# Optimization experiments

Measured on AMD Instinct MI355X. Metric: run time of the kernel, lower is better.

## Reference

```python
import jax, jax.numpy as jnp
import numpy as np

DIM = 1024
NUM_HEADS = 16
NUM_KV_HEADS = 4
HEAD_DIM = DIM // NUM_HEADS  # 64
QK_GAIN = 1.5
ROPE_BASE = 10000.0


def _rms_norm(x, eps):
    # F.rms_norm with no weight: x / sqrt(mean(x^2) + eps)
    ms = jnp.mean(jnp.square(x), axis=-1, keepdims=True)
    return x * jax.lax.rsqrt(ms + eps)


def _rope_tables(seqlen, dim, dtype):
    inv_freq = 1.0 / (ROPE_BASE ** (jnp.arange(0, dim, 2, dtype=jnp.float32) / dim))
    freqs = jnp.outer(jnp.arange(seqlen, dtype=jnp.float32), inv_freq)  # [N, D/2]
    emb = jnp.concatenate([freqs, freqs], axis=-1)  # [N, D]
    return jnp.cos(emb).astype(dtype), jnp.sin(emb).astype(dtype)


def _apply_rope(x, cos, sin):
    # x: [B, N, H, D]; cos/sin: [N, D] broadcast over batch and heads
    half = x.shape[-1] // 2
    rot = jnp.concatenate([-x[..., half:], x[..., :half]], axis=-1)
    return x * cos[None, :, None, :] + rot * sin[None, :, None, :]


def setup_inputs() -> dict:
    key = jax.random.key(0)
    ks = jax.random.split(key, 5)
    B, N, C = 4, 2048, DIM
    s = 0.02
    return {
        "x": jax.random.normal(ks[0], (B, N, C), dtype=jnp.float32),
        "wq": jax.random.normal(ks[1], (C, C), dtype=jnp.float32) * s,
        "wk": jax.random.normal(ks[2], (C, NUM_KV_HEADS * HEAD_DIM), dtype=jnp.float32) * s,
        "wv": jax.random.normal(ks[3], (C, NUM_KV_HEADS * HEAD_DIM), dtype=jnp.float32) * s,
        "wo": jax.random.normal(ks[4], (C, C), dtype=jnp.float32) * s,
    }


def reference(x, wq, wk, wv, wo) -> jnp.ndarray:
    B, N, C = x.shape
    H, Hkv, D = NUM_HEADS, NUM_KV_HEADS, HEAD_DIM
    eps = jnp.finfo(x.dtype).eps

    q = (x @ wq).reshape(B, N, H, D)
    k = (x @ wk).reshape(B, N, Hkv, D)
    v = (x @ wv).reshape(B, N, Hkv, D)

    q = _rms_norm(q, eps)
    k = _rms_norm(k, eps)

    cos, sin = _rope_tables(N, D, q.dtype)
    q = _apply_rope(q, cos, sin) * QK_GAIN
    k = _apply_rope(k, cos, sin)

    # GQA head expansion (repeat_interleave along head dim)
    g = H // Hkv
    k = jnp.repeat(k, g, axis=2)  # [B, N, H, D]
    v = jnp.repeat(v, g, axis=2)

    # causal SDPA, scale = 1/sqrt(D)
    scores = jnp.einsum("bqhd,bkhd->bhqk", q, k) / jnp.sqrt(jnp.asarray(D, q.dtype))
    causal = jnp.tril(jnp.ones((N, N), dtype=bool))
    scores = jnp.where(causal[None, None], scores, jnp.finfo(scores.dtype).min)
    probs = jax.nn.softmax(scores, axis=-1)
    y = jnp.einsum("bhqk,bkhd->bqhd", probs, v).reshape(B, N, C)
    return y @ wo
```

## Files before the change

### kernel.cpp

```cpp
#include <hip/hip_runtime.h>

typedef __bf16 bf16;
typedef __bf16 bf16x8 __attribute__((ext_vector_type(8)));
typedef __bf16 bf16x4 __attribute__((ext_vector_type(4)));
typedef float f32x4 __attribute__((ext_vector_type(4)));

#define B_ 4
#define N_ 2048
#define C_ 1024
#define H_ 16
#define HKV_ 4
#define D_ 64

#define QSCALE 0.2705053201666806f
#define NEGINF (-1.0e30f)

__global__ __launch_bounds__(256) void prep_qkv(const float* __restrict__ wq,
                                                const float* __restrict__ wk,
                                                const float* __restrict__ wv,
                                                bf16* __restrict__ wT) {
  __shared__ __align__(16) bf16 lds[64 * 72];
  int bx = blockIdx.x;
  const float* w;
  int ncols, tk, tn, nbase;
  if (bx < 256) {
    w = wq; ncols = 1024; tk = bx >> 4; tn = bx & 15; nbase = 0;
  } else if (bx < 320) {
    int t = bx - 256;
    w = wk; ncols = 256; tk = t >> 2; tn = t & 3; nbase = 1024;
  } else {
    int t = bx - 320;
    w = wv; ncols = 256; tk = t >> 2; tn = t & 3; nbase = 1280;
  }
  int tid = threadIdx.x;
#pragma unroll
  for (int i = 0; i < 4; ++i) {
    int c = tid + i * 256;
    int kr = c >> 4, n4 = (c & 15) * 4;
    f32x4 v = *(const f32x4*)(w + (size_t)(tk * 64 + kr) * ncols + tn * 64 + n4);
    bf16x4 b;
#pragma unroll
    for (int j = 0; j < 4; ++j) b[j] = (bf16)v[j];
    *(bf16x4*)(lds + kr * 72 + n4) = b;
  }
  __syncthreads();
#pragma unroll
  for (int i = 0; i < 2; ++i) {
    int c = tid + i * 256;
    int n = c >> 3, koff = (c & 7) * 8;
    bf16x8 tv;
#pragma unroll
    for (int j = 0; j < 8; ++j) tv[j] = lds[(koff + j) * 72 + n];
    *(bf16x8*)(wT + (size_t)(nbase + tn * 64 + n) * 1024 + tk * 64 + koff) = tv;
  }
}

__global__ __launch_bounds__(256) void prep_wo(const float* __restrict__ w,
                                               bf16* __restrict__ wT) {
  __shared__ __align__(16) bf16 lds[64 * 72];
  int tk = blockIdx.x >> 4, tn = blockIdx.x & 15;
  int tid = threadIdx.x;
#pragma unroll
  for (int i = 0; i < 4; ++i) {
    int c = tid + i * 256;
    int kr = c >> 4, n4 = (c & 15) * 4;
    f32x4 v = *(const f32x4*)(w + (size_t)(tk * 64 + kr) * 1024 + tn * 64 + n4);
    bf16x4 b;
#pragma unroll
    for (int j = 0; j < 4; ++j) b[j] = (bf16)v[j];
    *(bf16x4*)(lds + kr * 72 + n4) = b;
  }
  __syncthreads();
#pragma unroll
  for (int i = 0; i < 2; ++i) {
    int c = tid + i * 256;
    int n = c >> 3, koff = (c & 7) * 8;
    bf16x8 tv;
#pragma unroll
    for (int j = 0; j < 8; ++j) tv[j] = lds[(koff + j) * 72 + n];
    *(bf16x8*)(wT + (size_t)(tn * 64 + n) * 1024 + tk * 64 + koff) = tv;
  }
}

__global__ __launch_bounds__(256) void gemm_qkv(const float* __restrict__ x,
                                                const bf16* __restrict__ wT,
                                                bf16* __restrict__ qb,
                                                bf16* __restrict__ kvb) {
  __shared__ __align__(16) bf16 As[128 * 72];
  __shared__ __align__(16) bf16 Bs[128 * 72];
  int by = blockIdx.y;
  int n0 = by * 128;
  bf16* Out;
  int ostride, ocol0;
  if (by < 8) {
    Out = qb; ostride = 1024; ocol0 = by * 128;
  } else if (by < 10) {
    Out = kvb; ostride = 512; ocol0 = (by - 8) * 128;
  } else {
    Out = kvb; ostride = 512; ocol0 = 256 + (by - 10) * 128;
  }
  int m0 = blockIdx.x * 128;
  int tid = threadIdx.x;
  int wave = tid >> 6, lane = tid & 63;
  int quad = lane >> 4, lr = lane & 15;
  int wr = (wave >> 1) * 64, wc = (wave & 1) * 64;
  int arow = tid >> 4, aoff = (tid & 15) * 4;
  int brow = tid >> 3, boff = (tid & 7) * 8;

  f32x4 acc[4][4];
  const f32x4 z = {0.f, 0.f, 0.f, 0.f};
#pragma unroll
  for (int i = 0; i < 4; ++i)
#pragma unroll
    for (int j = 0; j < 4; ++j) acc[i][j] = z;

  f32x4 sa[8];
  bf16x8 sb[4];
#pragma unroll
  for (int i = 0; i < 8; ++i)
    sa[i] = *(const f32x4*)(x + (size_t)(m0 + arow + i * 16) * 1024 + aoff);
#pragma unroll
  for (int i = 0; i < 4; ++i)
    sb[i] = *(const bf16x8*)(wT + (size_t)(n0 + brow + i * 32) * 1024 + boff);
#pragma unroll
  for (int i = 0; i < 8; ++i) {
    bf16x4 a16;
#pragma unroll
    for (int j = 0; j < 4; ++j) a16[j] = (bf16)sa[i][j];
    *(bf16x4*)(As + (arow + i * 16) * 72 + aoff) = a16;
  }
#pragma unroll
  for (int i = 0; i < 4; ++i) *(bf16x8*)(Bs + (brow + i * 32) * 72 + boff) = sb[i];
  asm volatile("s_waitcnt lgkmcnt(0)" ::: "memory");
  __builtin_amdgcn_s_barrier();
  __builtin_amdgcn_sched_barrier(0);

  for (int k0 = 0; k0 < 1024; k0 += 64) {
    bool pf = (k0 + 64 < 1024);
    if (pf) {
#pragma unroll
      for (int i = 0; i < 8; ++i)
        sa[i] = *(const f32x4*)(x + (size_t)(m0 + arow + i * 16) * 1024 + k0 + 64 + aoff);
#pragma unroll
      for (int i = 0; i < 4; ++i)
        sb[i] = *(const bf16x8*)(wT + (size_t)(n0 + brow + i * 32) * 1024 + k0 + 64 + boff);
    }
#pragma unroll
    for (int kx = 0; kx < 2; ++kx) {
      bf16x8 af[4], bfr[4];
#pragma unroll
      for (int t = 0; t < 4; ++t) {
        af[t] = *(const bf16x8*)(As + (wr + t * 16 + lr) * 72 + kx * 32 + quad * 8);
        bfr[t] = *(const bf16x8*)(Bs + (wc + t * 16 + lr) * 72 + kx * 32 + quad * 8);
      }
      __builtin_amdgcn_s_setprio(1);
#pragma unroll
      for (int rt = 0; rt < 4; ++rt)
#pragma unroll
        for (int ct = 0; ct < 4; ++ct)
          acc[rt][ct] = __builtin_amdgcn_mfma_f32_16x16x32_bf16(af[rt], bfr[ct],
                                                                acc[rt][ct], 0, 0, 0);
      __builtin_amdgcn_s_setprio(0);
    }
    __builtin_amdgcn_s_barrier();
    __builtin_amdgcn_sched_barrier(0);
    if (pf) {
#pragma unroll
      for (int i = 0; i < 8; ++i) {
        bf16x4 a16;
#pragma unroll
        for (int j = 0; j < 4; ++j) a16[j] = (bf16)sa[i][j];
        *(bf16x4*)(As + (arow + i * 16) * 72 + aoff) = a16;
      }
#pragma unroll
      for (int i = 0; i < 4; ++i) *(bf16x8*)(Bs + (brow + i * 32) * 72 + boff) = sb[i];
      asm volatile("s_waitcnt lgkmcnt(0)" ::: "memory");
    }
    __builtin_amdgcn_s_barrier();
    __builtin_amdgcn_sched_barrier(0);
  }
#pragma unroll
  for (int rt = 0; rt < 4; ++rt)
#pragma unroll
    for (int ct = 0; ct < 4; ++ct)
#pragma unroll
      for (int r = 0; r < 4; ++r) {
        int row = m0 + wr + rt * 16 + quad * 4 + r;
        int col = ocol0 + wc + ct * 16 + lr;
        Out[(size_t)row * ostride + col] = (bf16)acc[rt][ct][r];
      }
}

__global__ __launch_bounds__(256) void gemm_out(const bf16* __restrict__ A,
                                                const bf16* __restrict__ Bt,
                                                float* __restrict__ C) {
  __shared__ __align__(16) bf16 As[128 * 72];
  __shared__ __align__(16) bf16 Bs[128 * 72];
  int m0 = blockIdx.x * 128, n0 = blockIdx.y * 128;
  int tid = threadIdx.x;
  int wave = tid >> 6, lane = tid & 63;
  int quad = lane >> 4, lr = lane & 15;
  int wr = (wave >> 1) * 64, wc = (wave & 1) * 64;
  int brow = tid >> 3, boff = (tid & 7) * 8;

  f32x4 acc[4][4];
  const f32x4 z = {0.f, 0.f, 0.f, 0.f};
#pragma unroll
  for (int i = 0; i < 4; ++i)
#pragma unroll
    for (int j = 0; j < 4; ++j) acc[i][j] = z;

  bf16x8 sa[4], sb[4];
#pragma unroll
  for (int i = 0; i < 4; ++i) {
    sa[i] = *(const bf16x8*)(A + (size_t)(m0 + brow + i * 32) * 1024 + boff);
    sb[i] = *(const bf16x8*)(Bt + (size_t)(n0 + brow + i * 32) * 1024 + boff);
  }
#pragma unroll
  for (int i = 0; i < 4; ++i) {
    *(bf16x8*)(As + (brow + i * 32) * 72 + boff) = sa[i];
    *(bf16x8*)(Bs + (brow + i * 32) * 72 + boff) = sb[i];
  }
  asm volatile("s_waitcnt lgkmcnt(0)" ::: "memory");
  __builtin_amdgcn_s_barrier();
  __builtin_amdgcn_sched_barrier(0);

  for (int k0 = 0; k0 < 1024; k0 += 64) {
    bool pf = (k0 + 64 < 1024);
    if (pf) {
#pragma unroll
      for (int i = 0; i < 4; ++i) {
        sa[i] = *(const bf16x8*)(A + (size_t)(m0 + brow + i * 32) * 1024 + k0 + 64 + boff);
        sb[i] = *(const bf16x8*)(Bt + (size_t)(n0 + brow + i * 32) * 1024 + k0 + 64 + boff);
      }
    }
#pragma unroll
    for (int kx = 0; kx < 2; ++kx) {
      bf16x8 af[4], bfr[4];
#pragma unroll
      for (int t = 0; t < 4; ++t) {
        af[t] = *(const bf16x8*)(As + (wr + t * 16 + lr) * 72 + kx * 32 + quad * 8);
        bfr[t] = *(const bf16x8*)(Bs + (wc + t * 16 + lr) * 72 + kx * 32 + quad * 8);
      }
      __builtin_amdgcn_s_setprio(1);
#pragma unroll
      for (int rt = 0; rt < 4; ++rt)
#pragma unroll
        for (int ct = 0; ct < 4; ++ct)
          acc[rt][ct] = __builtin_amdgcn_mfma_f32_16x16x32_bf16(af[rt], bfr[ct],
                                                                acc[rt][ct], 0, 0, 0);
      __builtin_amdgcn_s_setprio(0);
    }
    __builtin_amdgcn_s_barrier();
    __builtin_amdgcn_sched_barrier(0);
    if (pf) {
#pragma unroll
      for (int i = 0; i < 4; ++i) {
        *(bf16x8*)(As + (brow + i * 32) * 72 + boff) = sa[i];
        *(bf16x8*)(Bs + (brow + i * 32) * 72 + boff) = sb[i];
      }
      asm volatile("s_waitcnt lgkmcnt(0)" ::: "memory");
    }
    __builtin_amdgcn_s_barrier();
    __builtin_amdgcn_sched_barrier(0);
  }
#pragma unroll
  for (int rt = 0; rt < 4; ++rt)
#pragma unroll
    for (int ct = 0; ct < 4; ++ct)
#pragma unroll
      for (int r = 0; r < 4; ++r) {
        int row = m0 + wr + rt * 16 + quad * 4 + r;
        int col = n0 + wc + ct * 16 + lr;
        C[(size_t)row * 1024 + col] = acc[rt][ct][r];
      }
}

__global__ __launch_bounds__(256) void transpose_v(const bf16* __restrict__ kv,
                                                   bf16* __restrict__ vt) {
  __shared__ __align__(16) bf16 lds[64 * 72];
  int nt = blockIdx.x;
  int bh = blockIdx.y;
  int b = bh >> 2, hkv = bh & 3;
  int tid = threadIdx.x;
#pragma unroll
  for (int i = 0; i < 2; ++i) {
    int c = tid + i * 256;
    int tok = c >> 3, off = (c & 7) * 8;
    *(bf16x8*)(lds + tok * 72 + off) =
        *(const bf16x8*)(kv + (size_t)(b * N_ + nt * 64 + tok) * 512 + 256 + hkv * 64 + off);
  }
  __syncthreads();
#pragma unroll
  for (int i = 0; i < 2; ++i) {
    int c = tid + i * 256;
    int d = c >> 3, toff = (c & 7) * 8;
    bf16x8 tv;
#pragma unroll
    for (int j = 0; j < 8; ++j) tv[j] = lds[(toff + j) * 72 + d];
    *(bf16x8*)(vt + ((size_t)bh * 64 + d) * N_ + nt * 64 + toff) = tv;
  }
}

__global__ __launch_bounds__(256) void norm_rope(bf16* __restrict__ q,
                                                 bf16* __restrict__ kv) {
  int tid = threadIdx.x;
  int g = (blockIdx.x << 5) + (tid >> 3);
  int e = tid & 7;
  int t = g / 20;
  int sub = g - t * 20;
  int n = t & (N_ - 1);
  bf16* ptr;
  float oscale;
  if (sub < 16) {
    ptr = q + (size_t)t * 1024 + sub * 64;
    oscale = QSCALE;
  } else {
    ptr = kv + (size_t)t * 512 + (sub - 16) * 64;
    oscale = 1.0f;
  }
  bf16x8 v = *(const bf16x8*)(ptr + e * 8);
  float xv[8];
  float ss = 0.f;
#pragma unroll
  for (int i = 0; i < 8; ++i) {
    xv[i] = (float)v[i];
    ss += xv[i] * xv[i];
  }
  ss += __shfl_xor(ss, 1);
  ss += __shfl_xor(ss, 2);
  ss += __shfl_xor(ss, 4);
  float rn = rsqrtf(ss * (1.0f / 64.0f) + 1.1920929e-07f);
  float base = (float)((e & 3) * 8);
  bf16x8 o;
#pragma unroll
  for (int i = 0; i < 8; ++i) {
    float xn = xv[i] * rn;
    float pr = __shfl_xor(xn, 4);
    float rot = (e < 4) ? -pr : pr;
    float ang = (float)n * exp2f(-0.41524101186092029f * (base + (float)i));
    float sv, cv;
    __sincosf(ang, &sv, &cv);
    o[i] = (bf16)((xn * cv + rot * sv) * oscale);
  }
  *(bf16x8*)(ptr + e * 8) = o;
}

__global__ __launch_bounds__(256) void attn(bf16* __restrict__ q,
                                            const bf16* __restrict__ kv,
                                            const bf16* __restrict__ vt) {
  __shared__ __align__(16) bf16 Ks[2][64 * 64];
  __shared__ __align__(16) bf16 Vs[2][64 * 64];
  __shared__ __align__(16) bf16 Ps[64 * 64];
  int bid = blockIdx.x;
  int orig = (bid & 7) * 128 + (bid >> 3);
  int grp = orig >> 6;
  int inner = orig & 63;
  int b = grp >> 2, hkv = grp & 3;
  int h = hkv * 4 + (inner & 3);
  int p = inner >> 2;
  int tid = threadIdx.x;
  int wave = tid >> 6, lane = tid & 63;
  int quad = lane >> 4, lr = lane & 15;
  int srow = tid >> 3, soff = (tid & 7) * 8;
  int su = ((tid & 7) ^ (srow & 7)) * 8;
  int e7 = lr & 7;
  const f32x4 z = {0.f, 0.f, 0.f, 0.f};

#pragma unroll 1
  for (int s = 0; s < 2; ++s) {
    int j = s ? (31 - p) : p;
    __syncthreads();
    int qrow0 = j * 64 + wave * 16;
    int nkt = j + 1;

    bf16x8 qf[2];
#pragma unroll
    for (int kx = 0; kx < 2; ++kx)
      qf[kx] = *(const bf16x8*)(
          q + ((size_t)(b * N_ + qrow0 + lr) * H_ + h) * D_ + kx * 32 + quad * 8);

    f32x4 acc[4];
    float l_i = 0.f;
#pragma unroll
    for (int dt = 0; dt < 4; ++dt) acc[dt] = z;

    const bf16* kp = kv + (size_t)(b * N_ + srow) * 512 + hkv * 64 + soff;
    const bf16* vp = vt + ((size_t)(b * HKV_ + hkv) * 64 + srow) * N_ + soff;

    bf16x8 sk0, sk1, sv0, sv1;
    sk0 = *(const bf16x8*)(kp);
    sk1 = *(const bf16x8*)(kp + 32 * 512);
    sv0 = *(const bf16x8*)(vp);
    sv1 = *(const bf16x8*)(vp + 32 * N_);
    *(bf16x8*)(Ks[0] + srow * 64 + su) = sk0;
    *(bf16x8*)(Ks[0] + (srow + 32) * 64 + su) = sk1;
    *(bf16x8*)(Vs[0] + srow * 64 + su) = sv0;
    *(bf16x8*)(Vs[0] + (srow + 32) * 64 + su) = sv1;
    if (nkt > 1) {
      kp += 64 * 512;
      vp += 64;
      sk0 = *(const bf16x8*)(kp);
      sk1 = *(const bf16x8*)(kp + 32 * 512);
      sv0 = *(const bf16x8*)(vp);
      sv1 = *(const bf16x8*)(vp + 32 * N_);
    }
    asm volatile("s_waitcnt lgkmcnt(0)" ::: "memory");
    __builtin_amdgcn_s_barrier();
    __builtin_amdgcn_sched_barrier(0);

    int cur = 0;
    for (int kt = 0; kt < nkt; ++kt) {
      const bf16* Kc = Ks[cur];
      const bf16* Vc = Vs[cur];
      f32x4 st[4];
#pragma unroll
      for (int ct = 0; ct < 4; ++ct) st[ct] = z;
#pragma unroll
      for (int kx = 0; kx < 2; ++kx) {
        bf16x8 kf[4];
#pragma unroll
        for (int ct = 0; ct < 4; ++ct)
          kf[ct] = *(const bf16x8*)(Kc + (ct * 16 + lr) * 64 + (((kx * 4 + quad) ^ e7) * 8));
        __builtin_amdgcn_s_setprio(1);
#pragma unroll
        for (int ct = 0; ct < 4; ++ct)
          st[ct] = __builtin_amdgcn_mfma_f32_16x16x32_bf16(kf[ct], qf[kx], st[ct], 0, 0, 0);
        __builtin_amdgcn_s_setprio(0);
      }
      if (kt == j) {
        int qrow = qrow0 + lr;
#pragma unroll
        for (int ct = 0; ct < 4; ++ct)
#pragma unroll
          for (int r = 0; r < 4; ++r) {
            int key = kt * 64 + ct * 16 + quad * 4 + r;
            if (key > qrow) st[ct][r] = NEGINF;
          }
      }
      float rs = 0.f;
#pragma unroll
      for (int ct = 0; ct < 4; ++ct)
#pragma unroll
        for (int r = 0; r < 4; ++r) {
          float pv = exp2f(st[ct][r]);
          st[ct][r] = pv;
          rs += pv;
        }
      rs += __shfl_xor(rs, 16);
      rs += __shfl_xor(rs, 32);
      l_i += rs;
#pragma unroll
      for (int ct = 0; ct < 4; ++ct) {
        bf16x4 pk;
#pragma unroll
        for (int r = 0; r < 4; ++r) pk[r] = (bf16)st[ct][r];
        int pu = (((ct * 2) + (quad >> 1)) ^ e7) * 8 + (quad & 1) * 4;
        *(bf16x4*)(Ps + (wave * 16 + lr) * 64 + pu) = pk;
      }
      asm volatile("s_waitcnt lgkmcnt(0)" ::: "memory");
#pragma unroll
      for (int kx = 0; kx < 2; ++kx) {
        bf16x8 vf[4], pfr;
#pragma unroll
        for (int dt = 0; dt < 4; ++dt)
          vf[dt] = *(const bf16x8*)(Vc + (dt * 16 + lr) * 64 + (((kx * 4 + quad) ^ e7) * 8));
        pfr = *(const bf16x8*)(Ps + (wave * 16 + lr) * 64 + (((kx * 4 + quad) ^ e7) * 8));
        __builtin_amdgcn_s_setprio(1);
#pragma unroll
        for (int dt = 0; dt < 4; ++dt)
          acc[dt] = __builtin_amdgcn_mfma_f32_16x16x32_bf16(vf[dt], pfr, acc[dt], 0, 0, 0);
        __builtin_amdgcn_s_setprio(0);
      }

      bool pf = (kt + 1 < nkt);
      if (pf) {
        bf16* Kn = Ks[cur ^ 1];
        bf16* Vn = Vs[cur ^ 1];
        *(bf16x8*)(Kn + srow * 64 + su) = sk0;
        *(bf16x8*)(Kn + (srow + 32) * 64 + su) = sk1;
        *(bf16x8*)(Vn + srow * 64 + su) = sv0;
        *(bf16x8*)(Vn + (srow + 32) * 64 + su) = sv1;
        if (kt + 2 < nkt) {
          kp += 64 * 512;
          vp += 64;
          sk0 = *(const bf16x8*)(kp);
          sk1 = *(const bf16x8*)(kp + 32 * 512);
          sv0 = *(const bf16x8*)(vp);
          sv1 = *(const bf16x8*)(vp + 32 * N_);
        }
        asm volatile("s_waitcnt lgkmcnt(0)" ::: "memory");
      }
      __builtin_amdgcn_s_barrier();
      __builtin_amdgcn_sched_barrier(0);
      cur ^= 1;
    }

    float inv = 1.0f / l_i;
    int qrow = qrow0 + lr;
#pragma unroll
    for (int dt = 0; dt < 4; ++dt) {
      bf16x4 ov;
#pragma unroll
      for (int r = 0; r < 4; ++r) ov[r] = (bf16)(acc[dt][r] * inv);
      *(bf16x4*)(q + ((size_t)(b * N_ + qrow) * H_ + h) * D_ + dt * 16 + quad * 4) = ov;
    }
  }
}

extern "C" void kernel_launch(void* const* d_in, const int* in_sizes, int n_in,
                              void* d_out, int out_size, void* d_ws, size_t ws_size,
                              hipStream_t stream) {
  const float* x = (const float*)d_in[0];
  const float* wq = (const float*)d_in[1];
  const float* wk = (const float*)d_in[2];
  const float* wv = (const float*)d_in[3];
  const float* wo = (const float*)d_in[4];
  float* out = (float*)d_out;
  char* ws = (char*)d_ws;
  bf16* q = (bf16*)(ws);
  bf16* kv = (bf16*)(ws + 16777216);
  bf16* vt = (bf16*)(ws + 25165824);
  bf16* wqkvT = (bf16*)(ws + 25165824);
  bf16* woT = (bf16*)(ws + 25165824);

  prep_qkv<<<dim3(384), 256, 0, stream>>>(wq, wk, wv, wqkvT);
  gemm_qkv<<<dim3(64, 12), 256, 0, stream>>>(x, wqkvT, q, kv);
  norm_rope<<<dim3(5120), 256, 0, stream>>>(q, kv);
  transpose_v<<<dim3(32, 16), 256, 0, stream>>>(kv, vt);
  attn<<<dim3(1024), 256, 0, stream>>>(q, kv, vt);
  prep_wo<<<dim3(256), 256, 0, stream>>>(wo, woT);
  gemm_out<<<dim3(64, 8), 256, 0, stream>>>(q, woT, out);
}
```

Before: 255.3 us.

## Fuse RMS norm, RoPE and V transpose into QKV GEMM epilogue

Moves the per-head RMS normalization and rotary embedding for Q and K into the QKV GEMM epilogue, using shuffles across the 16-lane column group and pairing columns ct and ct^2 for the rotation. The V projection tiles are written transposed directly into the vt buffer, and K gets its own compact 256-stride buffer. This removes the norm_rope and transpose_v kernels, two launches and their extra global read/write passes, at the cost of heavier epilogue math and scattered 8-byte transposed V stores.

```diff
diff --git a/kernel.cpp b/kernel.cpp
--- a/kernel.cpp
+++ b/kernel.cpp
@@ -14,6 +14,7 @@
 
 #define QSCALE 0.2705053201666806f
 #define NEGINF (-1.0e30f)
+#define ROPE_C (-0.41524101186092029f)
 
 __global__ __launch_bounds__(256) void prep_qkv(const float* __restrict__ wq,
                                                 const float* __restrict__ wk,
@@ -85,20 +86,12 @@
 __global__ __launch_bounds__(256) void gemm_qkv(const float* __restrict__ x,
                                                 const bf16* __restrict__ wT,
                                                 bf16* __restrict__ qb,
-                                                bf16* __restrict__ kvb) {
+                                                bf16* __restrict__ kvK,
+                                                bf16* __restrict__ vt) {
   __shared__ __align__(16) bf16 As[128 * 72];
   __shared__ __align__(16) bf16 Bs[128 * 72];
   int by = blockIdx.y;
   int n0 = by * 128;
-  bf16* Out;
-  int ostride, ocol0;
-  if (by < 8) {
-    Out = qb; ostride = 1024; ocol0 = by * 128;
-  } else if (by < 10) {
-    Out = kvb; ostride = 512; ocol0 = (by - 8) * 128;
-  } else {
-    Out = kvb; ostride = 512; ocol0 = 256 + (by - 10) * 128;
-  }
   int m0 = blockIdx.x * 128;
   int tid = threadIdx.x;
   int wave = tid >> 6, lane = tid & 63;
@@ -179,16 +172,63 @@
     __builtin_amdgcn_s_barrier();
     __builtin_amdgcn_sched_barrier(0);
   }
-#pragma unroll
-  for (int rt = 0; rt < 4; ++rt)
-#pragma unroll
-    for (int ct = 0; ct < 4; ++ct)
+
+  if (by < 10) {
+    bf16* Out;
+    int ostride, ocol0;
+    float oscale;
+    if (by < 8) {
+      Out = qb; ostride = 1024; ocol0 = by * 128; oscale = QSCALE;
+    } else {
+      Out = kvK; ostride = 256; ocol0 = (by - 8) * 128; oscale = 1.0f;
+    }
+    float if0 = exp2f(ROPE_C * (float)lr);
+    float if1 = exp2f(ROPE_C * (float)(16 + lr));
+#pragma unroll
+    for (int rt = 0; rt < 4; ++rt) {
 #pragma unroll
       for (int r = 0; r < 4; ++r) {
+        float ss = 0.f;
+#pragma unroll
+        for (int ct = 0; ct < 4; ++ct) ss += acc[rt][ct][r] * acc[rt][ct][r];
+        ss += __shfl_xor(ss, 1);
+        ss += __shfl_xor(ss, 2);
+        ss += __shfl_xor(ss, 4);
+        ss += __shfl_xor(ss, 8);
+        float rn = rsqrtf(ss * (1.0f / 64.0f) + 1.1920929e-07f);
         int row = m0 + wr + rt * 16 + quad * 4 + r;
-        int col = ocol0 + wc + ct * 16 + lr;
-        Out[(size_t)row * ostride + col] = (bf16)acc[rt][ct][r];
-      }
+        float fn = (float)(row & (N_ - 1));
+        float sv0, cv0, sv1, cv1;
+        __sincosf(fn * if0, &sv0, &cv0);
+        __sincosf(fn * if1, &sv1, &cv1);
+#pragma unroll
+        for (int ct = 0; ct < 4; ++ct) {
+          float xn = acc[rt][ct][r] * rn;
+          float xp = acc[rt][ct ^ 2][r] * rn;
+          float rot = (ct < 2) ? -xp : xp;
+          float sv = (ct & 1) ? sv1 : sv0;
+          float cv = (ct & 1) ? cv1 : cv0;
+          int col = ocol0 + wc + ct * 16 + lr;
+          Out[(size_t)row * ostride + col] = (bf16)((xn * cv + rot * sv) * oscale);
+        }
+      }
+    }
+  } else {
+    int b = m0 >> 11;
+    int tokb = (m0 & (N_ - 1)) + wr;
+    int hv = (by - 10) * 2 + (wc >> 6);
+#pragma unroll
+    for (int rt = 0; rt < 4; ++rt)
+#pragma unroll
+      for (int ct = 0; ct < 4; ++ct) {
+        bf16x4 ov;
+#pragma unroll
+        for (int r = 0; r < 4; ++r) ov[r] = (bf16)acc[rt][ct][r];
+        int d = ct * 16 + lr;
+        int tok = tokb + rt * 16 + quad * 4;
+        *(bf16x4*)(vt + ((size_t)((b * 4 + hv) * 64 + d)) * N_ + tok) = ov;
+      }
+  }
 }
 
 __global__ __launch_bounds__(256) void gemm_out(const bf16* __restrict__ A,
@@ -274,76 +314,6 @@
         int col = n0 + wc + ct * 16 + lr;
         C[(size_t)row * 1024 + col] = acc[rt][ct][r];
       }
-}
-
-__global__ __launch_bounds__(256) void transpose_v(const bf16* __restrict__ kv,
-                                                   bf16* __restrict__ vt) {
-  __shared__ __align__(16) bf16 lds[64 * 72];
-  int nt = blockIdx.x;
-  int bh = blockIdx.y;
-  int b = bh >> 2, hkv = bh & 3;
-  int tid = threadIdx.x;
-#pragma unroll
-  for (int i = 0; i < 2; ++i) {
-    int c = tid + i * 256;
-    int tok = c >> 3, off = (c & 7) * 8;
-    *(bf16x8*)(lds + tok * 72 + off) =
-        *(const bf16x8*)(kv + (size_t)(b * N_ + nt * 64 + tok) * 512 + 256 + hkv * 64 + off);
-  }
-  __syncthreads();
-#pragma unroll
-  for (int i = 0; i < 2; ++i) {
-    int c = tid + i * 256;
-    int d = c >> 3, toff = (c & 7) * 8;
-    bf16x8 tv;
-#pragma unroll
-    for (int j = 0; j < 8; ++j) tv[j] = lds[(toff + j) * 72 + d];
-    *(bf16x8*)(vt + ((size_t)bh * 64 + d) * N_ + nt * 64 + toff) = tv;
-  }
-}
-
-__global__ __launch_bounds__(256) void norm_rope(bf16* __restrict__ q,
-                                                 bf16* __restrict__ kv) {
-  int tid = threadIdx.x;
-  int g = (blockIdx.x << 5) + (tid >> 3);
-  int e = tid & 7;
-  int t = g / 20;
-  int sub = g - t * 20;
-  int n = t & (N_ - 1);
-  bf16* ptr;
-  float oscale;
-  if (sub < 16) {
-    ptr = q + (size_t)t * 1024 + sub * 64;
-    oscale = QSCALE;
-  } else {
-    ptr = kv + (size_t)t * 512 + (sub - 16) * 64;
-    oscale = 1.0f;
-  }
-  bf16x8 v = *(const bf16x8*)(ptr + e * 8);
-  float xv[8];
-  float ss = 0.f;
-#pragma unroll
-  for (int i = 0; i < 8; ++i) {
-    xv[i] = (float)v[i];
-    ss += xv[i] * xv[i];
-  }
-  ss += __shfl_xor(ss, 1);
-  ss += __shfl_xor(ss, 2);
-  ss += __shfl_xor(ss, 4);
-  float rn = rsqrtf(ss * (1.0f / 64.0f) + 1.1920929e-07f);
-  float base = (float)((e & 3) * 8);
-  bf16x8 o;
-#pragma unroll
-  for (int i = 0; i < 8; ++i) {
-    float xn = xv[i] * rn;
-    float pr = __shfl_xor(xn, 4);
-    float rot = (e < 4) ? -pr : pr;
-    float ang = (float)n * exp2f(-0.41524101186092029f * (base + (float)i));
-    float sv, cv;
-    __sincosf(ang, &sv, &cv);
-    o[i] = (bf16)((xn * cv + rot * sv) * oscale);
-  }
-  *(bf16x8*)(ptr + e * 8) = o;
 }
 
 __global__ __launch_bounds__(256) void attn(bf16* __restrict__ q,
@@ -385,12 +355,12 @@
 #pragma unroll
     for (int dt = 0; dt < 4; ++dt) acc[dt] = z;
 
-    const bf16* kp = kv + (size_t)(b * N_ + srow) * 512 + hkv * 64 + soff;
+    const bf16* kp = kv + (size_t)(b * N_ + srow) * 256 + hkv * 64 + soff;
     const bf16* vp = vt + ((size_t)(b * HKV_ + hkv) * 64 + srow) * N_ + soff;
 
     bf16x8 sk0, sk1, sv0, sv1;
     sk0 = *(const bf16x8*)(kp);
-    sk1 = *(const bf16x8*)(kp + 32 * 512);
+    sk1 = *(const bf16x8*)(kp + 32 * 256);
     sv0 = *(const bf16x8*)(vp);
     sv1 = *(const bf16x8*)(vp + 32 * N_);
     *(bf16x8*)(Ks[0] + srow * 64 + su) = sk0;
@@ -398,10 +368,10 @@
     *(bf16x8*)(Vs[0] + srow * 64 + su) = sv0;
     *(bf16x8*)(Vs[0] + (srow + 32) * 64 + su) = sv1;
     if (nkt > 1) {
-      kp += 64 * 512;
+      kp += 64 * 256;
       vp += 64;
       sk0 = *(const bf16x8*)(kp);
-      sk1 = *(const bf16x8*)(kp + 32 * 512);
+      sk1 = *(const bf16x8*)(kp + 32 * 256);
       sv0 = *(const bf16x8*)(vp);
       sv1 = *(const bf16x8*)(vp + 32 * N_);
     }
@@ -482,10 +452,10 @@
         *(bf16x8*)(Vn + srow * 64 + su) = sv0;
         *(bf16x8*)(Vn + (srow + 32) * 64 + su) = sv1;
         if (kt + 2 < nkt) {
-          kp += 64 * 512;
+          kp += 64 * 256;
           vp += 64;
           sk0 = *(const bf16x8*)(kp);
-          sk1 = *(const bf16x8*)(kp + 32 * 512);
+          sk1 = *(const bf16x8*)(kp + 32 * 256);
           sv0 = *(const bf16x8*)(vp);
           sv1 = *(const bf16x8*)(vp + 32 * N_);
         }
@@ -519,16 +489,14 @@
   float* out = (float*)d_out;
   char* ws = (char*)d_ws;
   bf16* q = (bf16*)(ws);
-  bf16* kv = (bf16*)(ws + 16777216);
-  bf16* vt = (bf16*)(ws + 25165824);
+  bf16* kvK = (bf16*)(ws + 16777216);
+  bf16* vt = (bf16*)(ws + 20971520);
   bf16* wqkvT = (bf16*)(ws + 25165824);
   bf16* woT = (bf16*)(ws + 25165824);
 
   prep_qkv<<<dim3(384), 256, 0, stream>>>(wq, wk, wv, wqkvT);
-  gemm_qkv<<<dim3(64, 12), 256, 0, stream>>>(x, wqkvT, q, kv);
-  norm_rope<<<dim3(5120), 256, 0, stream>>>(q, kv);
-  transpose_v<<<dim3(32, 16), 256, 0, stream>>>(kv, vt);
-  attn<<<dim3(1024), 256, 0, stream>>>(q, kv, vt);
+  gemm_qkv<<<dim3(64, 12), 256, 0, stream>>>(x, wqkvT, q, kvK, vt);
+  attn<<<dim3(1024), 256, 0, stream>>>(q, kvK, vt);
   prep_wo<<<dim3(256), 256, 0, stream>>>(wo, woT);
   gemm_out<<<dim3(64, 8), 256, 0, stream>>>(q, woT, out);
 }
```

After: 234.3 us. 8.2% less time.
